# Optimization experiments

Hardware: AMD Instinct MI355X
Metric: run time of the kernel (lower is better)

Reference implementation:

```python
import jax, jax.numpy as jnp
import numpy as np

NUM_HEADS = 16
EPS = 1e-6

def _rmsnorm(h, w):
    h32 = h.astype(jnp.float32)
    var = jnp.mean(h32 * h32, axis=-1, keepdims=True)
    return (w * (h32 * jax.lax.rsqrt(var + EPS))).astype(h.dtype)

def setup_inputs() -> dict:
    key = jax.random.key(0)
    ks = jax.random.split(key, 4)
    B, N, C = 16, 1024, 1024
    x = jax.random.normal(ks[0], (B, N, C), dtype=jnp.float32)
    qkv_w = jax.random.normal(ks[1], (3 * C, C), dtype=jnp.float32) * (C ** -0.5)
    proj_w = jax.random.normal(ks[2], (C, C), dtype=jnp.float32) * (C ** -0.5)
    proj_b = jnp.zeros((C,), dtype=jnp.float32)
    q_norm_w = jnp.ones((C // NUM_HEADS,), dtype=jnp.float32)
    k_norm_w = jnp.ones((C // NUM_HEADS,), dtype=jnp.float32)
    return {"x": x, "qkv_w": qkv_w, "proj_w": proj_w, "proj_b": proj_b,
            "q_norm_w": q_norm_w, "k_norm_w": k_norm_w}

def reference(x, qkv_w, proj_w, proj_b, q_norm_w, k_norm_w):
    B, N, C = x.shape
    H = NUM_HEADS
    Dh = C // H
    scale = Dh ** -0.5  # qk_scale default; temperature = 1.0
    # QKV projection (no bias): [B,N,3,H,Dh]
    qkv = (x @ qkv_w.T).reshape(B, N, 3, H, Dh)
    q, k, v = qkv[:, :, 0], qkv[:, :, 1], qkv[:, :, 2]
    # per-head QK RMSNorm (fp32 internally)
    q = _rmsnorm(q, q_norm_w)
    k = _rmsnorm(k, k_norm_w)
    # explicit softmax attention: [B,H,N,N]
    attn = jnp.einsum('bnhd,bmhd->bhnm', q * scale, k)
    attn = jax.nn.softmax(attn, axis=-1)
    out = jnp.einsum('bhnm,bmhd->bnhd', attn, v).reshape(B, N, C)
    return out @ proj_w.T + proj_b
```

## Files before the change

kernel.cpp:

```cpp
#include <hip/hip_runtime.h>
#include <hip/hip_bf16.h>

typedef __attribute__((ext_vector_type(8))) __bf16 bf16x8;
typedef __attribute__((ext_vector_type(4))) __bf16 bf16x4;
typedef __attribute__((ext_vector_type(4))) float f32x4;

#define AS1(p) ((__attribute__((address_space(1))) void*)(p))
#define AS3(p) ((__attribute__((address_space(3))) void*)(p))

__global__ void f2b_kernel(const float4* __restrict__ in, bf16x4* __restrict__ out, int n4) {
    int idx = blockIdx.x * blockDim.x + threadIdx.x;
    int stride = gridDim.x * blockDim.x;
    for (int i = idx; i < n4; i += stride) {
        float4 v = in[i];
        bf16x4 o;
        o[0] = (__bf16)v.x; o[1] = (__bf16)v.y; o[2] = (__bf16)v.z; o[3] = (__bf16)v.w;
        out[i] = o;
    }
}

template<int MODE>
__global__ __launch_bounds__(512, 2)
void gemm256(const __bf16* __restrict__ A, const __bf16* __restrict__ Bw,
             const float* __restrict__ bias, const float* __restrict__ qw,
             const float* __restrict__ kw, float* __restrict__ Cf,
             __bf16* __restrict__ Cb, __bf16* __restrict__ Vt,
             int M, int K, int nbn, int ldc)
{
    __shared__ __bf16 Asl[4][256 * 32];
    __shared__ __bf16 Bsl[4][256 * 32];
    const int tid = threadIdx.x, l = tid & 63, w = tid >> 6;
    const int fr = l & 15, fk = l >> 4;

    const int cpx = gridDim.x >> 3;
    const int wg = (blockIdx.x & 7) * cpx + (blockIdx.x >> 3);
    const int bm = wg / nbn, bn = wg % nbn;

    const __bf16* Ag = A + (size_t)bm * 256 * K;
    const __bf16* Bg = Bw + (size_t)bn * 256 * K;

    const int arow = tid >> 2;
    const int uch = (tid & 3) ^ ((arow >> 1) & 3);
    const size_t ga = (size_t)arow * K + uch * 8;
    const size_t ga2 = ga + (size_t)128 * K;

    const int axc = (fk ^ ((fr >> 1) & 3)) * 16;
    int aoff[8], boff[4];
    #pragma unroll
    for (int m = 0; m < 8; ++m)
        aoff[m] = ((w >> 2) * 128 + m * 16 + fr) * 64 + axc;
    #pragma unroll
    for (int n = 0; n < 4; ++n)
        boff[n] = ((w & 3) * 64 + n * 16 + fr) * 64 + axc;

    f32x4 acc[8][4] = {};

#define STAGE256(S) do {                                                                    \
    const int sb_ = (S) & 3;                                                                \
    __builtin_amdgcn_global_load_lds(AS1(Ag + (size_t)(S) * 32 + ga),                       \
        AS3((char*)&Asl[sb_][0] + tid * 16), 16, 0, 0);                                     \
    __builtin_amdgcn_global_load_lds(AS1(Ag + (size_t)(S) * 32 + ga2),                      \
        AS3((char*)&Asl[sb_][0] + tid * 16 + 8192), 16, 0, 0);                              \
    __builtin_amdgcn_global_load_lds(AS1(Bg + (size_t)(S) * 32 + ga),                       \
        AS3((char*)&Bsl[sb_][0] + tid * 16), 16, 0, 0);                                     \
    __builtin_amdgcn_global_load_lds(AS1(Bg + (size_t)(S) * 32 + ga2),                      \
        AS3((char*)&Bsl[sb_][0] + tid * 16 + 8192), 16, 0, 0);                              \
} while (0)

#define PHASE256(S, VMSTR, DOSTAGE) do {                                                    \
    asm volatile("s_waitcnt vmcnt(" VMSTR ")" ::: "memory");                                \
    __builtin_amdgcn_s_barrier();                                                           \
    __builtin_amdgcn_sched_barrier(0);                                                      \
    const int pb_ = (S) & 3;                                                                \
    bf16x8 af[8], bfv[4];                                                                   \
    _Pragma("unroll")                                                                       \
    for (int m = 0; m < 8; ++m)                                                             \
        af[m] = *(const bf16x8*)((const char*)&Asl[pb_][0] + aoff[m]);                      \
    _Pragma("unroll")                                                                       \
    for (int n = 0; n < 4; ++n)                                                             \
        bfv[n] = *(const bf16x8*)((const char*)&Bsl[pb_][0] + boff[n]);                     \
    if (DOSTAGE) STAGE256((S) + 3);                                                         \
    __builtin_amdgcn_s_setprio(1);                                                          \
    _Pragma("unroll")                                                                       \
    for (int m = 0; m < 8; ++m)                                                             \
        _Pragma("unroll")                                                                   \
        for (int n = 0; n < 4; ++n)                                                         \
            acc[m][n] = __builtin_amdgcn_mfma_f32_16x16x32_bf16(af[m], bfv[n], acc[m][n], 0, 0, 0); \
    __builtin_amdgcn_s_setprio(0);                                                          \
} while (0)

    const int S = K >> 5;
    STAGE256(0); STAGE256(1); STAGE256(2);
    for (int s = 0; s < S - 2; ++s)
        PHASE256(s, "8", (s + 3 < S));
    PHASE256(S - 2, "4", false);
    PHASE256(S - 1, "0", false);
#undef PHASE256
#undef STAGE256

    const int rb0 = bm * 256 + (w >> 2) * 128 + fk * 4;
    const int cb0 = bn * 256 + (w & 3) * 64;

    if (MODE == 1) {
        #pragma unroll
        for (int m = 0; m < 8; ++m)
            #pragma unroll
            for (int n = 0; n < 4; ++n) {
                const int col = cb0 + n * 16 + fr;
                const float bv = bias[col];
                #pragma unroll
                for (int r = 0; r < 4; ++r)
                    Cf[(size_t)(rb0 + m * 16 + r) * ldc + col] = acc[m][n][r] + bv;
            }
    } else {
        const int sect = bn >> 2;
        if (sect < 2) {
            const float* wp = (sect == 0) ? qw : kw;
            float wn[4];
            #pragma unroll
            for (int n = 0; n < 4; ++n) wn[n] = wp[((w & 3) * 64 + n * 16 + fr) & 63];
            #pragma unroll
            for (int m = 0; m < 8; ++m) {
                float sc[4];
                #pragma unroll
                for (int r = 0; r < 4; ++r) {
                    float ps = 0.f;
                    #pragma unroll
                    for (int n = 0; n < 4; ++n) ps += acc[m][n][r] * acc[m][n][r];
                    ps += __shfl_xor(ps, 1); ps += __shfl_xor(ps, 2);
                    ps += __shfl_xor(ps, 4); ps += __shfl_xor(ps, 8);
                    sc[r] = rsqrtf(ps * (1.0f / 64.0f) + 1e-6f);
                    if (sect == 0) sc[r] *= 0.18033688011112042f;
                }
                #pragma unroll
                for (int n = 0; n < 4; ++n)
                    #pragma unroll
                    for (int r = 0; r < 4; ++r)
                        Cb[(size_t)(rb0 + m * 16 + r) * ldc + cb0 + n * 16 + fr] =
                            (__bf16)(acc[m][n][r] * sc[r] * wn[n]);
            }
        } else {
            #pragma unroll
            for (int m = 0; m < 8; ++m) {
                const int tok = rb0 + m * 16;
                const int b = tok >> 10, ntok = tok & 1023;
                #pragma unroll
                for (int n = 0; n < 4; ++n) {
                    const int vd = (bn - 8) * 256 + (w & 3) * 64 + n * 16 + fr;
                    bf16x4 pk;
                    #pragma unroll
                    for (int r = 0; r < 4; ++r) pk[r] = (__bf16)acc[m][n][r];
                    *(bf16x4*)&Vt[((size_t)((b * 16 + (vd >> 6)) * 64 + (vd & 63))) * 1024 + ntok] = pk;
                }
            }
        }
    }
}

__global__ __launch_bounds__(256, 2)
void attn_kernel(const __bf16* __restrict__ qkv, const __bf16* __restrict__ vt,
                 __bf16* __restrict__ ao)
{
    __shared__ __bf16 Ks[2][64 * 64];
    __shared__ __bf16 Vs[2][64 * 64];
    __shared__ __bf16 Pl[4][16 * 64];
    const int tid = threadIdx.x, l = tid & 63, w = tid >> 6;
    const int fr = l & 15, fk = l >> 4;
    const int sw = (fr & 7) << 4;

    const int bi = blockIdx.x;
    const int L = (bi & 7) * 128 + (bi >> 3);
    const int qb = L & 3, h = (L >> 2) & 15, b = L >> 6;

    const __bf16* Kg = qkv + (size_t)b * 1024 * 2048 + 1024 + h * 64;
    const __bf16* Vg = vt + (size_t)((b * 16 + h) * 64) * 1024;
    const int srow = tid >> 3, scp = tid & 7;

    const int c8 = (scp ^ (srow & 7)) * 8;
    const size_t kO0 = (size_t)srow * 2048 + c8, kO1 = kO0 + 32 * 2048;
    const size_t vO0 = (size_t)srow * 1024 + c8, vO1 = vO0 + 32 * 1024;
    char* ksd = (char*)&Ks[0][0] + tid * 16;
    char* vsd = (char*)&Vs[0][0] + tid * 16;

#define STAGE(KP, VP, BUF) do {                                                           \
    __builtin_amdgcn_global_load_lds(AS1((KP) + kO0), AS3(ksd + (BUF) * 8192), 16, 0, 0); \
    __builtin_amdgcn_global_load_lds(AS1((KP) + kO1), AS3(ksd + (BUF) * 8192 + 4096), 16, 0, 0); \
    __builtin_amdgcn_global_load_lds(AS1((VP) + vO0), AS3(vsd + (BUF) * 8192), 16, 0, 0); \
    __builtin_amdgcn_global_load_lds(AS1((VP) + vO1), AS3(vsd + (BUF) * 8192 + 4096), 16, 0, 0); \
} while (0)

    STAGE(Kg, Vg, 0);

    const int qrow0 = b * 1024 + qb * 256 + w * 64;
    bf16x8 qf[4][2];
    #pragma unroll
    for (int qi = 0; qi < 4; ++qi)
        #pragma unroll
        for (int dc = 0; dc < 2; ++dc)
            qf[qi][dc] = *(const bf16x8*)&qkv[(size_t)(qrow0 + qi * 16 + fr) * 2048
                                              + h * 64 + dc * 32 + fk * 8];

    const int kb0 = fr * 128 + ((fk ^ (fr & 7)) * 16);
    const int kb1 = fr * 128 + (((4 + fk) ^ (fr & 7)) * 16);
    const char* KsB = (const char*)&Ks[0][0];
    const char* VsB = (const char*)&Vs[0][0];

    char* Pw = (char*)&Pl[w][0];
    const int pw0 = (fr * 128 + 0 * 32 + fk * 8) ^ sw;
    const int pw1 = (fr * 128 + 1 * 32 + fk * 8) ^ sw;
    const int pw2 = (fr * 128 + 2 * 32 + fk * 8) ^ sw;
    const int pw3 = (fr * 128 + 3 * 32 + fk * 8) ^ sw;
    const int pr0 = (fr * 128 + 0 * 64 + fk * 16) ^ sw;
    const int pr1 = (fr * 128 + 1 * 64 + fk * 16) ^ sw;

    bf16x8 onesf;
    #pragma unroll
    for (int i = 0; i < 8; ++i) onesf[i] = (__bf16)1.0f;

    f32x4 oacc[4][4] = {};
    f32x4 lacc[4] = {};

    const __bf16* kg = Kg;
    const __bf16* vg = Vg;
    __syncthreads();

    for (int kt = 0; kt < 16; ++kt) {
        const int cur = kt & 1;
        if (kt < 15) { kg += 64 * 2048; vg += 64; STAGE(kg, vg, cur ^ 1); }

        const int cb = cur * 8192;
        bf16x8 kf[4][2], vf[4][2];
        #pragma unroll
        for (int n = 0; n < 4; ++n) {
            kf[n][0] = *(const bf16x8*)(KsB + cb + kb0 + n * 2048);
            kf[n][1] = *(const bf16x8*)(KsB + cb + kb1 + n * 2048);
        }
        #pragma unroll
        for (int nd = 0; nd < 4; ++nd) {
            vf[nd][0] = *(const bf16x8*)(VsB + cb + kb0 + nd * 2048);
            vf[nd][1] = *(const bf16x8*)(VsB + cb + kb1 + nd * 2048);
        }

        #pragma unroll
        for (int qi = 0; qi < 4; ++qi) {
            f32x4 sacc[4] = {};
            #pragma unroll
            for (int n = 0; n < 4; ++n)
                #pragma unroll
                for (int dc = 0; dc < 2; ++dc)
                    sacc[n] = __builtin_amdgcn_mfma_f32_16x16x32_bf16(kf[n][dc], qf[qi][dc],
                                                                      sacc[n], 0, 0, 0);

            #pragma unroll
            for (int n = 0; n < 4; ++n) {
                bf16x4 pk;
                #pragma unroll
                for (int r = 0; r < 4; ++r)
                    pk[r] = (__bf16)__builtin_amdgcn_exp2f(sacc[n][r]);
                const int pwn = (n == 0) ? pw0 : (n == 1) ? pw1 : (n == 2) ? pw2 : pw3;
                *(bf16x4*)(Pw + pwn) = pk;
            }

            bf16x8 pf0 = *(const bf16x8*)(Pw + pr0);
            bf16x8 pf1 = *(const bf16x8*)(Pw + pr1);
            lacc[qi] = __builtin_amdgcn_mfma_f32_16x16x32_bf16(pf0, onesf, lacc[qi], 0, 0, 0);
            lacc[qi] = __builtin_amdgcn_mfma_f32_16x16x32_bf16(pf1, onesf, lacc[qi], 0, 0, 0);
            #pragma unroll
            for (int nd = 0; nd < 4; ++nd) {
                oacc[qi][nd] = __builtin_amdgcn_mfma_f32_16x16x32_bf16(pf0, vf[nd][0],
                                                                       oacc[qi][nd], 0, 0, 0);
                oacc[qi][nd] = __builtin_amdgcn_mfma_f32_16x16x32_bf16(pf1, vf[nd][1],
                                                                       oacc[qi][nd], 0, 0, 0);
            }
        }
        __syncthreads();
    }

    #pragma unroll
    for (int qi = 0; qi < 4; ++qi) {
        float inv[4];
        #pragma unroll
        for (int r = 0; r < 4; ++r)
            inv[r] = __builtin_amdgcn_rcpf(lacc[qi][r]);
        #pragma unroll
        for (int nd = 0; nd < 4; ++nd)
            #pragma unroll
            for (int r = 0; r < 4; ++r)
                ao[(size_t)(qrow0 + qi * 16 + fk * 4 + r) * 1024 + h * 64 + nd * 16 + fr] =
                    (__bf16)(oacc[qi][nd][r] * inv[r]);
    }
#undef STAGE
}

extern "C" void kernel_launch(void* const* d_in, const int* in_sizes, int n_in,
                              void* d_out, int out_size, void* d_ws, size_t ws_size,
                              hipStream_t stream)
{
    const float* x      = (const float*)d_in[0];
    const float* qkv_w  = (const float*)d_in[1];
    const float* proj_w = (const float*)d_in[2];
    const float* proj_b = (const float*)d_in[3];
    const float* qnw    = (const float*)d_in[4];
    const float* knw    = (const float*)d_in[5];

    char* ws = (char*)d_ws;
    __bf16* xb    = (__bf16*)(ws);
    __bf16* wqkv  = (__bf16*)(ws + 33554432);
    __bf16* wproj = (__bf16*)(ws + 39845888);
    __bf16* qkv   = (__bf16*)(ws + 41943040);
    __bf16* vt    = (__bf16*)(ws + 109051904);
    __bf16* ao    = (__bf16*)(ws + 142606336);

    f2b_kernel<<<2048, 256, 0, stream>>>((const float4*)x,      (bf16x4*)xb,    16777216 / 4);
    f2b_kernel<<<2048, 256, 0, stream>>>((const float4*)qkv_w,  (bf16x4*)wqkv,  3145728 / 4);
    f2b_kernel<<<1024, 256, 0, stream>>>((const float4*)proj_w, (bf16x4*)wproj, 1048576 / 4);

    gemm256<0><<<768, 512, 0, stream>>>(xb, wqkv, nullptr, qnw, knw,
                                        nullptr, qkv, vt, 16384, 1024, 12, 2048);
    attn_kernel<<<1024, 256, 0, stream>>>(qkv, vt, ao);
    gemm256<1><<<256, 512, 0, stream>>>(ao, wproj, proj_b, nullptr, nullptr,
                                        (float*)d_out, nullptr, nullptr, 16384, 1024, 4, 1024);
}
```

Baseline: 255.8 us.

## Stage two K/V tiles per barrier with four-buffer LDS ring in attention

Measured after the change: 254.1 us. About the same (-0.7%).

```diff
diff --git a/kernel.cpp b/kernel.cpp
--- a/kernel.cpp
+++ b/kernel.cpp
@@ -161,8 +161,8 @@
 void attn_kernel(const __bf16* __restrict__ qkv, const __bf16* __restrict__ vt,
                  __bf16* __restrict__ ao)
 {
-    __shared__ __bf16 Ks[2][64 * 64];
-    __shared__ __bf16 Vs[2][64 * 64];
+    __shared__ __bf16 Ks[4][64 * 64];
+    __shared__ __bf16 Vs[4][64 * 64];
     __shared__ __bf16 Pl[4][16 * 64];
     const int tid = threadIdx.x, l = tid & 63, w = tid >> 6;
     const int fr = l & 15, fk = l >> 4;
@@ -182,14 +182,16 @@
     char* ksd = (char*)&Ks[0][0] + tid * 16;
     char* vsd = (char*)&Vs[0][0] + tid * 16;
 
-#define STAGE(KP, VP, BUF) do {                                                           \
-    __builtin_amdgcn_global_load_lds(AS1((KP) + kO0), AS3(ksd + (BUF) * 8192), 16, 0, 0); \
-    __builtin_amdgcn_global_load_lds(AS1((KP) + kO1), AS3(ksd + (BUF) * 8192 + 4096), 16, 0, 0); \
-    __builtin_amdgcn_global_load_lds(AS1((VP) + vO0), AS3(vsd + (BUF) * 8192), 16, 0, 0); \
-    __builtin_amdgcn_global_load_lds(AS1((VP) + vO1), AS3(vsd + (BUF) * 8192 + 4096), 16, 0, 0); \
+#define STAGE(KT) do {                                                                    \
+    char* dk_ = ksd + ((KT) & 3) * 8192;                                                  \
+    char* dv_ = vsd + ((KT) & 3) * 8192;                                                  \
+    __builtin_amdgcn_global_load_lds(AS1(Kg + (size_t)(KT) * 131072 + kO0), AS3(dk_), 16, 0, 0); \
+    __builtin_amdgcn_global_load_lds(AS1(Kg + (size_t)(KT) * 131072 + kO1), AS3(dk_ + 4096), 16, 0, 0); \
+    __builtin_amdgcn_global_load_lds(AS1(Vg + (KT) * 64 + vO0), AS3(dv_), 16, 0, 0);      \
+    __builtin_amdgcn_global_load_lds(AS1(Vg + (KT) * 64 + vO1), AS3(dv_ + 4096), 16, 0, 0); \
 } while (0)
 
-    STAGE(Kg, Vg, 0);
+    STAGE(0); STAGE(1);
 
     const int qrow0 = b * 1024 + qb * 256 + w * 64;
     bf16x8 qf[4][2];
@@ -220,60 +222,60 @@
     f32x4 oacc[4][4] = {};
     f32x4 lacc[4] = {};
 
-    const __bf16* kg = Kg;
-    const __bf16* vg = Vg;
-    __syncthreads();
-
-    for (int kt = 0; kt < 16; ++kt) {
-        const int cur = kt & 1;
-        if (kt < 15) { kg += 64 * 2048; vg += 64; STAGE(kg, vg, cur ^ 1); }
-
-        const int cb = cur * 8192;
-        bf16x8 kf[4][2], vf[4][2];
-        #pragma unroll
-        for (int n = 0; n < 4; ++n) {
-            kf[n][0] = *(const bf16x8*)(KsB + cb + kb0 + n * 2048);
-            kf[n][1] = *(const bf16x8*)(KsB + cb + kb1 + n * 2048);
+    for (int p = 0; p < 8; ++p) {
+        asm volatile("s_waitcnt vmcnt(0)" ::: "memory");
+        __builtin_amdgcn_s_barrier();
+        __builtin_amdgcn_sched_barrier(0);
+        if (p < 7) { STAGE(2 * p + 2); STAGE(2 * p + 3); }
+
+        #pragma unroll
+        for (int kh = 0; kh < 2; ++kh) {
+            const int cb = (((p & 1) << 1) | kh) * 8192;
+            bf16x8 kf[4][2], vf[4][2];
+            #pragma unroll
+            for (int n = 0; n < 4; ++n) {
+                kf[n][0] = *(const bf16x8*)(KsB + cb + kb0 + n * 2048);
+                kf[n][1] = *(const bf16x8*)(KsB + cb + kb1 + n * 2048);
+            }
+            #pragma unroll
+            for (int nd = 0; nd < 4; ++nd) {
+                vf[nd][0] = *(const bf16x8*)(VsB + cb + kb0 + nd * 2048);
+                vf[nd][1] = *(const bf16x8*)(VsB + cb + kb1 + nd * 2048);
+            }
+
+            #pragma unroll
+            for (int qi = 0; qi < 4; ++qi) {
+                f32x4 sacc[4] = {};
+                #pragma unroll
+                for (int n = 0; n < 4; ++n)
+                    #pragma unroll
+                    for (int dc = 0; dc < 2; ++dc)
+                        sacc[n] = __builtin_amdgcn_mfma_f32_16x16x32_bf16(kf[n][dc], qf[qi][dc],
+                                                                          sacc[n], 0, 0, 0);
+
+                #pragma unroll
+                for (int n = 0; n < 4; ++n) {
+                    bf16x4 pk;
+                    #pragma unroll
+                    for (int r = 0; r < 4; ++r)
+                        pk[r] = (__bf16)__builtin_amdgcn_exp2f(sacc[n][r]);
+                    const int pwn = (n == 0) ? pw0 : (n == 1) ? pw1 : (n == 2) ? pw2 : pw3;
+                    *(bf16x4*)(Pw + pwn) = pk;
+                }
+
+                bf16x8 pf0 = *(const bf16x8*)(Pw + pr0);
+                bf16x8 pf1 = *(const bf16x8*)(Pw + pr1);
+                lacc[qi] = __builtin_amdgcn_mfma_f32_16x16x32_bf16(pf0, onesf, lacc[qi], 0, 0, 0);
+                lacc[qi] = __builtin_amdgcn_mfma_f32_16x16x32_bf16(pf1, onesf, lacc[qi], 0, 0, 0);
+                #pragma unroll
+                for (int nd = 0; nd < 4; ++nd) {
+                    oacc[qi][nd] = __builtin_amdgcn_mfma_f32_16x16x32_bf16(pf0, vf[nd][0],
+                                                                           oacc[qi][nd], 0, 0, 0);
+                    oacc[qi][nd] = __builtin_amdgcn_mfma_f32_16x16x32_bf16(pf1, vf[nd][1],
+                                                                           oacc[qi][nd], 0, 0, 0);
+                }
+            }
         }
-        #pragma unroll
-        for (int nd = 0; nd < 4; ++nd) {
-            vf[nd][0] = *(const bf16x8*)(VsB + cb + kb0 + nd * 2048);
-            vf[nd][1] = *(const bf16x8*)(VsB + cb + kb1 + nd * 2048);
-        }
-
-        #pragma unroll
-        for (int qi = 0; qi < 4; ++qi) {
-            f32x4 sacc[4] = {};
-            #pragma unroll
-            for (int n = 0; n < 4; ++n)
-                #pragma unroll
-                for (int dc = 0; dc < 2; ++dc)
-                    sacc[n] = __builtin_amdgcn_mfma_f32_16x16x32_bf16(kf[n][dc], qf[qi][dc],
-                                                                      sacc[n], 0, 0, 0);
-
-            #pragma unroll
-            for (int n = 0; n < 4; ++n) {
-                bf16x4 pk;
-                #pragma unroll
-                for (int r = 0; r < 4; ++r)
-                    pk[r] = (__bf16)__builtin_amdgcn_exp2f(sacc[n][r]);
-                const int pwn = (n == 0) ? pw0 : (n == 1) ? pw1 : (n == 2) ? pw2 : pw3;
-                *(bf16x4*)(Pw + pwn) = pk;
-            }
-
-            bf16x8 pf0 = *(const bf16x8*)(Pw + pr0);
-            bf16x8 pf1 = *(const bf16x8*)(Pw + pr1);
-            lacc[qi] = __builtin_amdgcn_mfma_f32_16x16x32_bf16(pf0, onesf, lacc[qi], 0, 0, 0);
-            lacc[qi] = __builtin_amdgcn_mfma_f32_16x16x32_bf16(pf1, onesf, lacc[qi], 0, 0, 0);
-            #pragma unroll
-            for (int nd = 0; nd < 4; ++nd) {
-                oacc[qi][nd] = __builtin_amdgcn_mfma_f32_16x16x32_bf16(pf0, vf[nd][0],
-                                                                       oacc[qi][nd], 0, 0, 0);
-                oacc[qi][nd] = __builtin_amdgcn_mfma_f32_16x16x32_bf16(pf1, vf[nd][1],
-                                                                       oacc[qi][nd], 0, 0, 0);
-            }
-        }
-        __syncthreads();
     }
 
     #pragma unroll
```
